# Optimization experiments

Hardware: AMD Instinct MI355X
Metric: run time of the kernel (lower is better)

The kernel has to match this reference:

```python
import jax, jax.numpy as jnp
import numpy as np

EPS = 1e-6

def setup_inputs() -> dict:
    key = jax.random.key(0)
    k1, k2, k3, k4, k5, k6 = jax.random.split(key, 6)
    B, S, N_IMG, D = 4, 4096, 2048, 2048
    encoder = jax.random.normal(k1, (B, S, D), dtype=jnp.float32)
    objectness = jax.random.normal(k2, (B, N_IMG), dtype=jnp.float32)
    boxes = jax.random.uniform(k3, (B, N_IMG, 4), dtype=jnp.float32)
    # learned parameters
    gamma = jnp.ones((D,), dtype=jnp.float32) + 0.02 * jax.random.normal(k4, (D,), dtype=jnp.float32)  # T5LayerNorm weight
    w = jax.random.normal(k5, (D,), dtype=jnp.float32) / np.sqrt(D)  # Linear(n_in, 1) weight, flattened
    b = jax.random.normal(k6, (), dtype=jnp.float32) * 0.01          # Linear bias
    return {"encoder": encoder, "objectness": objectness, "boxes": boxes,
            "gamma": gamma, "w": w, "b": b}

def reference(encoder, objectness, boxes, gamma, w, b):
    # n_images = boxes.shape[1]; slice candidate regions
    n_images = boxes.shape[1]
    x = encoder[:, :n_images]                                  # [B, n_images, D]
    # T5LayerNorm: RMS normalization (no mean subtraction), scale by gamma
    variance = jnp.mean(jnp.square(x), axis=-1, keepdims=True)  # [B, n_images, 1]
    x_norm = x * jax.lax.rsqrt(variance + EPS) * gamma          # [B, n_images, D]
    # Linear(D, 1) -> squeeze(-1): a GEMV over the feature axis
    image_rel = jnp.einsum('bnd,d->bn', x_norm, w) + b          # [B, n_images]
    return image_rel
```

## Files before the change

### kernel.cpp

```cpp
#include <hip/hip_runtime.h>

#define EPS 1e-6f

__global__ __launch_bounds__(256) void LinearObjectness_kernel(
    const float* __restrict__ enc,
    const float* __restrict__ gamma,
    const float* __restrict__ w,
    const float* __restrict__ bias,
    float* __restrict__ out,
    int N_IMG, int S, int D)
{
    const int row = blockIdx.x;
    const int b   = row / N_IMG;
    const int n   = row % N_IMG;
    const float* __restrict__ x = enc + ((size_t)b * S + n) * (size_t)D;

    const int t = threadIdx.x;

    float sumsq = 0.f;
    float dot   = 0.f;

    for (int base = 0; base < D; base += 1024) {
        const int idx = base + t * 4;
        const float4 xv = *reinterpret_cast<const float4*>(x + idx);
        const float4 gv = *reinterpret_cast<const float4*>(gamma + idx);
        const float4 wv = *reinterpret_cast<const float4*>(w + idx);
        sumsq += xv.x * xv.x + xv.y * xv.y + xv.z * xv.z + xv.w * xv.w;
        dot   += xv.x * gv.x * wv.x + xv.y * gv.y * wv.y
               + xv.z * gv.z * wv.z + xv.w * gv.w * wv.w;
    }

    #pragma unroll
    for (int o = 32; o > 0; o >>= 1) {
        sumsq += __shfl_down(sumsq, o, 64);
        dot   += __shfl_down(dot,   o, 64);
    }

    __shared__ float s_sq[4];
    __shared__ float s_dot[4];
    const int wid  = t >> 6;
    const int lane = t & 63;
    if (lane == 0) { s_sq[wid] = sumsq; s_dot[wid] = dot; }
    __syncthreads();

    if (t == 0) {
        const float ss  = s_sq[0] + s_sq[1] + s_sq[2] + s_sq[3];
        const float dd  = s_dot[0] + s_dot[1] + s_dot[2] + s_dot[3];
        const float inv = rsqrtf(ss / (float)D + EPS);
        out[row] = dd * inv + bias[0];
    }
}

extern "C" void kernel_launch(void* const* d_in, const int* in_sizes, int n_in,
                              void* d_out, int out_size, void* d_ws, size_t ws_size,
                              hipStream_t stream) {
    const float* enc   = (const float*)d_in[0];
    const float* gamma = (const float*)d_in[3];
    const float* w     = (const float*)d_in[4];
    const float* bias  = (const float*)d_in[5];
    float* out         = (float*)d_out;

    const int D     = in_sizes[3];
    const int B     = 4;
    const int BN    = in_sizes[1];
    const int N_IMG = BN / B;
    const int S     = in_sizes[0] / (B * D);

    LinearObjectness_kernel<<<BN, 256, 0, stream>>>(enc, gamma, w, bias, out,
                                                    N_IMG, S, D);
}
```

Baseline: 16.11 us.

## Map one wavefront per row with compile-time D and no shared-memory reduction

```diff
diff --git a/kernel.cpp b/kernel.cpp
--- a/kernel.cpp
+++ b/kernel.cpp
@@ -2,7 +2,52 @@
 
 #define EPS 1e-6f
 
-__global__ __launch_bounds__(256) void LinearObjectness_kernel(
+template<int D>
+__global__ __launch_bounds__(256, 4) void lo_kernel(
+    const float* __restrict__ enc,
+    const float* __restrict__ gamma,
+    const float* __restrict__ w,
+    const float* __restrict__ bias,
+    float* __restrict__ out,
+    int N_IMG, int S, int n_rows)
+{
+    const int lane = threadIdx.x & 63;
+    const int row  = blockIdx.x * 4 + (threadIdx.x >> 6);
+    if (row >= n_rows) return;
+
+    const int b = row / N_IMG;
+    const int n = row % N_IMG;
+    const float* __restrict__ x = enc + ((size_t)b * S + n) * (size_t)D;
+
+    constexpr int ITER = D / 256;
+
+    float sumsq = 0.f, dot = 0.f;
+    #pragma unroll
+    for (int i = 0; i < ITER; ++i) {
+        const int idx = i * 256 + lane * 4;
+        const float4 xv = *reinterpret_cast<const float4*>(x + idx);
+        const float4 gv = *reinterpret_cast<const float4*>(gamma + idx);
+        const float4 wv = *reinterpret_cast<const float4*>(w + idx);
+        sumsq = fmaf(xv.x, xv.x, fmaf(xv.y, xv.y, fmaf(xv.z, xv.z, fmaf(xv.w, xv.w, sumsq))));
+        dot  = fmaf(xv.x * gv.x, wv.x,
+               fmaf(xv.y * gv.y, wv.y,
+               fmaf(xv.z * gv.z, wv.z,
+               fmaf(xv.w * gv.w, wv.w, dot))));
+    }
+
+    #pragma unroll
+    for (int o = 32; o > 0; o >>= 1) {
+        sumsq += __shfl_xor(sumsq, o, 64);
+        dot   += __shfl_xor(dot,   o, 64);
+    }
+
+    if (lane == 0) {
+        const float inv = rsqrtf(sumsq * (1.0f / (float)D) + EPS);
+        out[row] = dot * inv + bias[0];
+    }
+}
+
+__global__ __launch_bounds__(256) void lo_kernel_generic(
     const float* __restrict__ enc,
     const float* __restrict__ gamma,
     const float* __restrict__ w,
@@ -14,40 +59,27 @@
     const int b   = row / N_IMG;
     const int n   = row % N_IMG;
     const float* __restrict__ x = enc + ((size_t)b * S + n) * (size_t)D;
-
     const int t = threadIdx.x;
 
-    float sumsq = 0.f;
-    float dot   = 0.f;
-
-    for (int base = 0; base < D; base += 1024) {
-        const int idx = base + t * 4;
-        const float4 xv = *reinterpret_cast<const float4*>(x + idx);
-        const float4 gv = *reinterpret_cast<const float4*>(gamma + idx);
-        const float4 wv = *reinterpret_cast<const float4*>(w + idx);
-        sumsq += xv.x * xv.x + xv.y * xv.y + xv.z * xv.z + xv.w * xv.w;
-        dot   += xv.x * gv.x * wv.x + xv.y * gv.y * wv.y
-               + xv.z * gv.z * wv.z + xv.w * gv.w * wv.w;
+    float sumsq = 0.f, dot = 0.f;
+    for (int d = t; d < D; d += 256) {
+        const float xv = x[d];
+        sumsq = fmaf(xv, xv, sumsq);
+        dot   = fmaf(xv * gamma[d], w[d], dot);
     }
-
     #pragma unroll
     for (int o = 32; o > 0; o >>= 1) {
-        sumsq += __shfl_down(sumsq, o, 64);
-        dot   += __shfl_down(dot,   o, 64);
+        sumsq += __shfl_xor(sumsq, o, 64);
+        dot   += __shfl_xor(dot,   o, 64);
     }
-
-    __shared__ float s_sq[4];
-    __shared__ float s_dot[4];
-    const int wid  = t >> 6;
-    const int lane = t & 63;
+    __shared__ float s_sq[4], s_dot[4];
+    const int wid = t >> 6, lane = t & 63;
     if (lane == 0) { s_sq[wid] = sumsq; s_dot[wid] = dot; }
     __syncthreads();
-
     if (t == 0) {
-        const float ss  = s_sq[0] + s_sq[1] + s_sq[2] + s_sq[3];
-        const float dd  = s_dot[0] + s_dot[1] + s_dot[2] + s_dot[3];
-        const float inv = rsqrtf(ss / (float)D + EPS);
-        out[row] = dd * inv + bias[0];
+        float ss = s_sq[0] + s_sq[1] + s_sq[2] + s_sq[3];
+        float dd = s_dot[0] + s_dot[1] + s_dot[2] + s_dot[3];
+        out[row] = dd * rsqrtf(ss / (float)D + EPS) + bias[0];
     }
 }
 
@@ -60,12 +92,19 @@
     const float* bias  = (const float*)d_in[5];
     float* out         = (float*)d_out;
 
-    const int D     = in_sizes[3];
-    const int B     = 4;
-    const int BN    = in_sizes[1];
-    const int N_IMG = BN / B;
-    const int S     = in_sizes[0] / (B * D);
+    const int D      = in_sizes[3];
+    const int B      = 4;
+    const int BN     = in_sizes[1];
+    const int N_IMG  = BN / B;
+    const int S      = in_sizes[0] / (B * D);
+    const int n_rows = out_size;
 
-    LinearObjectness_kernel<<<BN, 256, 0, stream>>>(enc, gamma, w, bias, out,
-                                                    N_IMG, S, D);
+    if (D == 2048) {
+        const int blocks = (n_rows + 3) / 4;
+        lo_kernel<2048><<<blocks, 256, 0, stream>>>(enc, gamma, w, bias, out,
+                                                    N_IMG, S, n_rows);
+    } else {
+        lo_kernel_generic<<<n_rows, 256, 0, stream>>>(enc, gamma, w, bias, out,
+                                                      N_IMG, S, D);
+    }
 }
```

Result: no change. 15.80 us (-2.0%).
